# Optimization experiments

Hardware: AMD Instinct MI355X
Metric: run time of the kernel (lower is better)

Reference implementation:

```python
import jax, jax.numpy as jnp
import numpy as np

N_PRED, B, N_NEG, D = 12, 256, 128, 512


def setup_inputs() -> dict:
    key = jax.random.key(0)
    k1, k2, k3, k4 = jax.random.split(key, 4)
    lp = jax.random.normal(k1, (N_PRED + 1, B, D), dtype=jnp.float32)  # [0]='k', [t]='k+t'
    ps = jax.random.normal(k2, (N_PRED, B, D), dtype=jnp.float32)      # [t-1]='k+t'
    # time index over the N_PRED+1 keys (0 -> 'k' from latent_predictions, j -> 'k+j' from positives)
    time_idx = jax.random.randint(k3, (N_PRED, B, N_NEG), 0, N_PRED + 1, dtype=jnp.int32)
    # batch index uniform over B-1 rows excluding self: draw in [0, B-1) then shift past own row
    r = jax.random.randint(k4, (N_PRED, B, N_NEG), 0, B - 1, dtype=jnp.int32)
    own = jnp.arange(B, dtype=jnp.int32)[None, :, None]
    batch_idx = r + (r >= own).astype(jnp.int32)
    return {"latent_predictions": lp, "positive_samples": ps,
            "time_idx": time_idx, "batch_idx": batch_idx}


def reference(latent_predictions, positive_samples, time_idx, batch_idx):
    lp, ps = latent_predictions, positive_samples
    # Negative-sample bank: index 0 = 'k' (from predictions), index j = 'k+j' (from positives)
    bank = jnp.concatenate([lp[:1], ps], axis=0)            # [N_PRED+1, B, D]
    negs = bank[time_idx, batch_idx]                         # [N_PRED, B, N_NEG, D]
    preds = lp[1:]                                           # [N_PRED, B, D]
    # f_k = sum_d exp(z_d * c_d)  (elementwise product, as in the original)
    fk_pos = jnp.sum(jnp.exp(preds * ps), axis=-1)                       # [N_PRED, B]
    fk_neg = jnp.sum(jnp.exp(preds[:, :, None, :] * negs), axis=-1)      # [N_PRED, B, N_NEG]
    per_step = jnp.log(fk_pos / (fk_pos + jnp.sum(fk_neg, axis=-1)))     # [N_PRED, B]
    loss_vec = jnp.sum(per_step, axis=0) / ((N_NEG + 1) * N_PRED)        # [B]
    loss = jnp.sum(loss_vec) / B
    correct_predictions = jnp.sum(
        jnp.all(fk_pos[:, :, None] > fk_neg, axis=-1).astype(jnp.float32), axis=1)  # [N_PRED]
    return loss, correct_predictions
```

## Files before the change

### kernel.cpp

```cpp
#include <hip/hip_runtime.h>
#include <hip/hip_fp16.h>
#include <math.h>

#define N_PRED 12
#define B      256
#define N_NEG  128
#define D      512
#define NROWS  ((N_PRED + 1) * B)
#define LOG2E  1.4426950408889634f
#define LN2    0.6931471805599453f

typedef float f2 __attribute__((ext_vector_type(2)));

__device__ __forceinline__ float ex2(float x) { return __builtin_amdgcn_exp2f(x); }

__global__ __launch_bounds__(256) void conv_kernel(
    const float* __restrict__ lp, const float* __restrict__ ps,
    __half* __restrict__ hbank)
{
    const int e8 = blockIdx.x * 256 + threadIdx.x;
    const int e  = e8 * 8;
    const float* src = (e < B * D) ? (lp + e) : (ps + (e - B * D));
    float4 a = ((const float4*)src)[0];
    float4 b = ((const float4*)src)[1];
    union { uint4 u; __half2 h[4]; } o;
    o.h[0] = __floats2half2_rn(a.x, a.y);
    o.h[1] = __floats2half2_rn(a.z, a.w);
    o.h[2] = __floats2half2_rn(b.x, b.y);
    o.h[3] = __floats2half2_rn(b.z, b.w);
    ((uint4*)hbank)[e8] = o.u;
}

__device__ __forceinline__ float fk_half(const __half* __restrict__ rowh,
                                         const f2* __restrict__ p2, int q) {
    const uint4* r = (const uint4*)rowh;
    f2 acc = {0.f, 0.f};
#pragma unroll
    for (int j = 0; j < 4; ++j) {
        uint4 w = r[q + 16 * j];
        const __half2* hp = (const __half2*)&w;
        float2 f0 = __half22float2(hp[0]);
        float2 f1 = __half22float2(hp[1]);
        float2 f2v = __half22float2(hp[2]);
        float2 f3 = __half22float2(hp[3]);
        f2 m0 = p2[4 * j + 0] * f2{f0.x, f0.y};
        f2 m1 = p2[4 * j + 1] * f2{f1.x, f1.y};
        f2 m2 = p2[4 * j + 2] * f2{f2v.x, f2v.y};
        f2 m3 = p2[4 * j + 3] * f2{f3.x, f3.y};
        acc += f2{ex2(m0.x), ex2(m0.y)};
        acc += f2{ex2(m1.x), ex2(m1.y)};
        acc += f2{ex2(m2.x), ex2(m2.y)};
        acc += f2{ex2(m3.x), ex2(m3.y)};
    }
    return acc.x + acc.y;
}

__global__ __launch_bounds__(256) void fk_kernel_h(
    const float* __restrict__ lp,
    const float* __restrict__ ps,
    const int*   __restrict__ time_idx,
    const int*   __restrict__ batch_idx,
    const __half* __restrict__ hbank,
    float* __restrict__ per_step,
    float* __restrict__ flags)
{
    const int tb   = blockIdx.x;
    const int t    = tb >> 8;
    const int b    = tb & (B - 1);
    const int tid  = threadIdx.x;
    const int wave = tid >> 6;
    const int lane = tid & 63;
    const int q    = lane & 15;
    const int g    = lane >> 4;

    __shared__ const __half* s_rowh[N_NEG];
    __shared__ const float*  s_row32[N_NEG];
    __shared__ float s_sum[4];
    __shared__ float s_max[4];
    __shared__ int   s_oki[4];
    __shared__ int   s_flag;

    const int idx_base = (t * B + b) * N_NEG;
    if (tid < N_NEG) {
        const int ti  = time_idx[idx_base + tid];
        const int bi  = batch_idx[idx_base + tid];
        const int rid = ti * B + bi;
        s_rowh[tid]  = hbank + (size_t)rid * D;
        s_row32[tid] = (ti == 0) ? (lp + (size_t)bi * D)
                                 : (ps + ((size_t)(ti - 1) * B + bi) * D);
    }

    const float4* pred4 = (const float4*)(lp + ((size_t)(t + 1) * B + b) * D);
    f2 p2[16];
#pragma unroll
    for (int j = 0; j < 4; ++j) {
        float4 pa = pred4[(q + 16 * j) * 2];
        float4 pb = pred4[(q + 16 * j) * 2 + 1];
        p2[4 * j + 0] = f2{pa.x * LOG2E, pa.y * LOG2E};
        p2[4 * j + 1] = f2{pa.z * LOG2E, pa.w * LOG2E};
        p2[4 * j + 2] = f2{pb.x * LOG2E, pb.y * LOG2E};
        p2[4 * j + 3] = f2{pb.z * LOG2E, pb.w * LOG2E};
    }

    float fk_pos;
    {
        float s = fk_half(hbank + ((size_t)(t + 1) * B + b) * D, p2, q);
#pragma unroll
        for (int off = 1; off < 16; off <<= 1) s += __shfl_xor(s, off, 64);
        fk_pos = s;
    }

    __syncthreads();

    float negsum = 0.0f;
    float maxfk  = 0.0f;

#pragma unroll 2
    for (int it = 0; it < 8; ++it) {
        const int n = wave * 32 + it * 4 + g;
        float fk = fk_half(s_rowh[n], p2, q);
#pragma unroll
        for (int off = 1; off < 16; off <<= 1) fk += __shfl_xor(fk, off, 64);
        negsum += fk;
        maxfk   = fmaxf(maxfk, fk);
    }

    float ns = negsum;
#pragma unroll
    for (int off = 16; off < 64; off <<= 1) ns += __shfl_xor(ns, off, 64);
    float mx = maxfk;
#pragma unroll
    for (int off = 16; off < 64; off <<= 1) mx = fmaxf(mx, __shfl_xor(mx, off, 64));

    if (lane == 0) { s_sum[wave] = ns; s_max[wave] = mx; }
    __syncthreads();
    if (tid == 0) {
        float total_neg = (s_sum[0] + s_sum[1]) + (s_sum[2] + s_sum[3]);
        float bmx = fmaxf(fmaxf(s_max[0], s_max[1]), fmaxf(s_max[2], s_max[3]));
        float total = fk_pos + total_neg;
        per_step[tb] = (__builtin_amdgcn_logf(fk_pos) - __builtin_amdgcn_logf(total)) * LN2;
        float margin = fk_pos - bmx;
        int near = fabsf(margin) <= 0.08f * fmaxf(fk_pos, bmx);
        s_flag = near;
        if (!near) flags[tb] = (margin > 0.0f) ? 1.0f : 0.0f;
    }
    __syncthreads();

    if (s_flag) {
        float4 pl0 = pred4[lane];
        float4 pl1 = pred4[lane + 64];
        pl0.x *= LOG2E; pl0.y *= LOG2E; pl0.z *= LOG2E; pl0.w *= LOG2E;
        pl1.x *= LOG2E; pl1.y *= LOG2E; pl1.z *= LOG2E; pl1.w *= LOG2E;

        const float4* pr = (const float4*)(ps + ((size_t)t * B + b) * D);
        float4 ya = pr[lane], yb = pr[lane + 64];
        float sp = ex2(pl0.x * ya.x) + ex2(pl0.y * ya.y) + ex2(pl0.z * ya.z) + ex2(pl0.w * ya.w)
                 + ex2(pl1.x * yb.x) + ex2(pl1.y * yb.y) + ex2(pl1.z * yb.z) + ex2(pl1.w * yb.w);
#pragma unroll
        for (int off = 1; off < 64; off <<= 1) sp += __shfl_xor(sp, off, 64);
        const float fkpos32 = sp;

        int okx = 1;
        for (int n = wave * 32; n < wave * 32 + 32; ++n) {
            const float4* r4 = (const float4*)s_row32[n];
            float4 za = r4[lane], zb = r4[lane + 64];
            float s = ex2(pl0.x * za.x) + ex2(pl0.y * za.y) + ex2(pl0.z * za.z) + ex2(pl0.w * za.w)
                    + ex2(pl1.x * zb.x) + ex2(pl1.y * zb.y) + ex2(pl1.z * zb.z) + ex2(pl1.w * zb.w);
#pragma unroll
            for (int off = 1; off < 64; off <<= 1) s += __shfl_xor(s, off, 64);
            okx &= (fkpos32 > s) ? 1 : 0;
        }
        if (lane == 0) s_oki[wave] = okx;
        __syncthreads();
        if (tid == 0)
            flags[tb] = (float)(s_oki[0] & s_oki[1] & s_oki[2] & s_oki[3]);
    }
}

__global__ __launch_bounds__(256) void fk_kernel_f32(
    const float* __restrict__ lp, const float* __restrict__ ps,
    const int* __restrict__ time_idx, const int* __restrict__ batch_idx,
    float* __restrict__ per_step, float* __restrict__ flags)
{
    const int tb   = blockIdx.x;
    const int t    = tb >> 8;
    const int b    = tb & (B - 1);
    const int tid  = threadIdx.x;
    const int wave = tid >> 6;
    const int lane = tid & 63;
    const int q    = lane & 15;
    const int g    = lane >> 4;

    __shared__ const float* s_row[N_NEG];
    __shared__ float s_sum[4];
    __shared__ int   s_ok[4];

    const int idx_base = (t * B + b) * N_NEG;
    if (tid < N_NEG) {
        const int ti = time_idx[idx_base + tid];
        const int bi = batch_idx[idx_base + tid];
        s_row[tid] = (ti == 0) ? (lp + (size_t)bi * D)
                               : (ps + ((size_t)(ti - 1) * B + bi) * D);
    }

    const float4* pred4 = (const float4*)(lp + ((size_t)(t + 1) * B + b) * D) + q;
    f2 p2[16];
#pragma unroll
    for (int j = 0; j < 8; ++j) {
        float4 v = pred4[j * 16];
        p2[2 * j]     = f2{v.x * LOG2E, v.y * LOG2E};
        p2[2 * j + 1] = f2{v.z * LOG2E, v.w * LOG2E};
    }

    float fk_pos;
    {
        const float4* pos4 = (const float4*)(ps + ((size_t)t * B + b) * D) + q;
        f2 acc = {0.f, 0.f};
#pragma unroll
        for (int j = 0; j < 8; ++j) {
            float4 y = pos4[j * 16];
            f2 m0 = p2[2 * j] * f2{y.x, y.y};
            f2 m1 = p2[2 * j + 1] * f2{y.z, y.w};
            acc += f2{ex2(m0.x), ex2(m0.y)};
            acc += f2{ex2(m1.x), ex2(m1.y)};
        }
        float s = acc.x + acc.y;
#pragma unroll
        for (int off = 1; off < 16; off <<= 1) s += __shfl_xor(s, off, 64);
        fk_pos = s;
    }

    __syncthreads();

    float negsum = 0.0f;
    bool  all_ok = true;
#pragma unroll 2
    for (int it = 0; it < 8; ++it) {
        const int n = wave * 32 + it * 4 + g;
        const float4* row4 = (const float4*)s_row[n] + q;
        f2 acc = {0.f, 0.f};
#pragma unroll
        for (int j = 0; j < 8; ++j) {
            float4 y = row4[j * 16];
            f2 m0 = p2[2 * j] * f2{y.x, y.y};
            f2 m1 = p2[2 * j + 1] * f2{y.z, y.w};
            acc += f2{ex2(m0.x), ex2(m0.y)};
            acc += f2{ex2(m1.x), ex2(m1.y)};
        }
        float fk = acc.x + acc.y;
#pragma unroll
        for (int off = 1; off < 16; off <<= 1) fk += __shfl_xor(fk, off, 64);
        negsum += fk;
        all_ok  = all_ok && (fk_pos > fk);
    }

    const int wave_ok = __all(all_ok ? 1 : 0);
    float ns = negsum;
#pragma unroll
    for (int off = 16; off < 64; off <<= 1) ns += __shfl_xor(ns, off, 64);

    if (lane == 0) { s_sum[wave] = ns; s_ok[wave] = wave_ok; }
    __syncthreads();
    if (tid == 0) {
        float total_neg = (s_sum[0] + s_sum[1]) + (s_sum[2] + s_sum[3]);
        int   ok        = s_ok[0] & s_ok[1] & s_ok[2] & s_ok[3];
        float total     = fk_pos + total_neg;
        per_step[tb] = (__builtin_amdgcn_logf(fk_pos) - __builtin_amdgcn_logf(total)) * LN2;
        flags[tb]    = (float)ok;
    }
}

__global__ __launch_bounds__(256) void reduce_kernel(
    const float* __restrict__ per_step,
    const float* __restrict__ flags,
    float* __restrict__ out)
{
    const int tid = threadIdx.x;
    const int j   = blockIdx.x;
    __shared__ float sh[4];

    float s = 0.0f;
    if (j == 0) {
#pragma unroll
        for (int t = 0; t < N_PRED; ++t) s += per_step[t * B + tid];
    } else {
        s = flags[(j - 1) * B + tid];
    }
#pragma unroll
    for (int off = 32; off > 0; off >>= 1) s += __shfl_xor(s, off, 64);
    if ((tid & 63) == 0) sh[tid >> 6] = s;
    __syncthreads();
    if (tid == 0) {
        float tot = (sh[0] + sh[1]) + (sh[2] + sh[3]);
        if (j == 0)
            out[0] = tot * (1.0f / ((float)(N_NEG + 1) * N_PRED * B));
        else
            out[j] = tot;
    }
}

extern "C" void kernel_launch(void* const* d_in, const int* in_sizes, int n_in,
                              void* d_out, int out_size, void* d_ws, size_t ws_size,
                              hipStream_t stream) {
    const float* lp        = (const float*)d_in[0];
    const float* ps        = (const float*)d_in[1];
    const int*   time_idx  = (const int*)d_in[2];
    const int*   batch_idx = (const int*)d_in[3];
    float* out = (float*)d_out;

    const size_t hbytes = (size_t)NROWS * D * sizeof(__half);
    const size_t need   = hbytes + 2 * (size_t)N_PRED * B * sizeof(float);

    if (ws_size >= need) {
        __half* hbank   = (__half*)d_ws;
        float* per_step = (float*)((char*)d_ws + hbytes);
        float* flags    = per_step + N_PRED * B;
        conv_kernel<<<NROWS * D / 8 / 256, 256, 0, stream>>>(lp, ps, hbank);
        fk_kernel_h<<<N_PRED * B, 256, 0, stream>>>(lp, ps, time_idx, batch_idx,
                                                    hbank, per_step, flags);
        reduce_kernel<<<1 + N_PRED, 256, 0, stream>>>(per_step, flags, out);
    } else {
        float* per_step = (float*)d_ws;
        float* flags    = per_step + N_PRED * B;
        fk_kernel_f32<<<N_PRED * B, 256, 0, stream>>>(lp, ps, time_idx, batch_idx,
                                                      per_step, flags);
        reduce_kernel<<<1 + N_PRED, 256, 0, stream>>>(per_step, flags, out);
    }
}
```

Baseline: 53.69 us.

## Stage gathered negative rows into per-wave LDS ring via async global-to-LDS loads

Replaces direct global loads of gathered fp16 negative rows with async global_load_lds copies into a per-wave 8-slot LDS ring buffer, prefetching the next group of four rows while computing the current one. The goal is to overlap gather latency with the exp/accumulate work. It adds about 33 KB of LDS per block, which may cut occupancy, and relies on manual vmcnt waits for correctness.

```diff
diff --git a/kernel.cpp b/kernel.cpp
--- a/kernel.cpp
+++ b/kernel.cpp
@@ -9,10 +9,18 @@
 #define NROWS  ((N_PRED + 1) * B)
 #define LOG2E  1.4426950408889634f
 #define LN2    0.6931471805599453f
+#define ROWB   1056
+#define RING   8
 
 typedef float f2 __attribute__((ext_vector_type(2)));
 
 __device__ __forceinline__ float ex2(float x) { return __builtin_amdgcn_exp2f(x); }
+
+__device__ __forceinline__ void ld_lds16(const void* g, void* l) {
+    __builtin_amdgcn_global_load_lds(
+        (const __attribute__((address_space(1))) void*)g,
+        (__attribute__((address_space(3))) void*)l, 16, 0, 0);
+}
 
 __global__ __launch_bounds__(256) void conv_kernel(
     const float* __restrict__ lp, const float* __restrict__ ps,
@@ -31,8 +39,8 @@
     ((uint4*)hbank)[e8] = o.u;
 }
 
-__device__ __forceinline__ float fk_half(const __half* __restrict__ rowh,
-                                         const f2* __restrict__ p2, int q) {
+__device__ __forceinline__ float fk_half_g(const __half* __restrict__ rowh,
+                                           const f2* __restrict__ p2, int q) {
     const uint4* r = (const uint4*)rowh;
     f2 acc = {0.f, 0.f};
 #pragma unroll
@@ -41,11 +49,34 @@
         const __half2* hp = (const __half2*)&w;
         float2 f0 = __half22float2(hp[0]);
         float2 f1 = __half22float2(hp[1]);
-        float2 f2v = __half22float2(hp[2]);
+        float2 fv = __half22float2(hp[2]);
         float2 f3 = __half22float2(hp[3]);
         f2 m0 = p2[4 * j + 0] * f2{f0.x, f0.y};
         f2 m1 = p2[4 * j + 1] * f2{f1.x, f1.y};
-        f2 m2 = p2[4 * j + 2] * f2{f2v.x, f2v.y};
+        f2 m2 = p2[4 * j + 2] * f2{fv.x, fv.y};
+        f2 m3 = p2[4 * j + 3] * f2{f3.x, f3.y};
+        acc += f2{ex2(m0.x), ex2(m0.y)};
+        acc += f2{ex2(m1.x), ex2(m1.y)};
+        acc += f2{ex2(m2.x), ex2(m2.y)};
+        acc += f2{ex2(m3.x), ex2(m3.y)};
+    }
+    return acc.x + acc.y;
+}
+
+__device__ __forceinline__ float fk_lds(const unsigned char* rowb,
+                                        const f2* __restrict__ p2, int q) {
+    f2 acc = {0.f, 0.f};
+#pragma unroll
+    for (int j = 0; j < 4; ++j) {
+        uint4 w = *(const uint4*)(rowb + q * 16 + j * 256);
+        const __half2* hp = (const __half2*)&w;
+        float2 f0 = __half22float2(hp[0]);
+        float2 f1 = __half22float2(hp[1]);
+        float2 fv = __half22float2(hp[2]);
+        float2 f3 = __half22float2(hp[3]);
+        f2 m0 = p2[4 * j + 0] * f2{f0.x, f0.y};
+        f2 m1 = p2[4 * j + 1] * f2{f1.x, f1.y};
+        f2 m2 = p2[4 * j + 2] * f2{fv.x, fv.y};
         f2 m3 = p2[4 * j + 3] * f2{f3.x, f3.y};
         acc += f2{ex2(m0.x), ex2(m0.y)};
         acc += f2{ex2(m1.x), ex2(m1.y)};
@@ -73,6 +104,7 @@
     const int q    = lane & 15;
     const int g    = lane >> 4;
 
+    __shared__ __align__(16) unsigned char s_ring[4][RING * ROWB];
     __shared__ const __half* s_rowh[N_NEG];
     __shared__ const float*  s_row32[N_NEG];
     __shared__ float s_sum[4];
@@ -104,7 +136,7 @@
 
     float fk_pos;
     {
-        float s = fk_half(hbank + ((size_t)(t + 1) * B + b) * D, p2, q);
+        float s = fk_half_g(hbank + ((size_t)(t + 1) * B + b) * D, p2, q);
 #pragma unroll
         for (int off = 1; off < 16; off <<= 1) s += __shfl_xor(s, off, 64);
         fk_pos = s;
@@ -112,13 +144,31 @@
 
     __syncthreads();
 
+    const int base = wave * 32;
+    unsigned char* ringw = &s_ring[wave][0];
+
+#pragma unroll
+    for (int jj = 0; jj < 4; ++jj)
+        ld_lds16((const char*)s_rowh[base + jj] + lane * 16, ringw + jj * ROWB);
+
     float negsum = 0.0f;
     float maxfk  = 0.0f;
 
-#pragma unroll 2
+#pragma unroll
     for (int it = 0; it < 8; ++it) {
-        const int n = wave * 32 + it * 4 + g;
-        float fk = fk_half(s_rowh[n], p2, q);
+        if (it < 7) {
+#pragma unroll
+            for (int jj = 0; jj < 4; ++jj)
+                ld_lds16((const char*)s_rowh[base + (it + 1) * 4 + jj] + lane * 16,
+                         ringw + (((it + 1) * 4 + jj) & 7) * ROWB);
+            asm volatile("s_waitcnt vmcnt(4)" ::: "memory");
+        } else {
+            asm volatile("s_waitcnt vmcnt(0)" ::: "memory");
+        }
+        __builtin_amdgcn_sched_barrier(0);
+
+        const unsigned char* rowb = ringw + (((it * 4 + g) & 7) * ROWB);
+        float fk = fk_lds(rowb, p2, q);
 #pragma unroll
         for (int off = 1; off < 16; off <<= 1) fk += __shfl_xor(fk, off, 64);
         negsum += fk;
```

Measured after the change: 56.55 us. +5.3%, slower.
